# Optimization experiments

Measured on AMD Instinct MI355X. Metric: run time of the kernel, lower is better.

Reference implementation:

```python
import jax, jax.numpy as jnp
from jax import lax
import numpy as np

SCALES = 3
DIR_PROFILE = [2, 3, 4]


def _gaussian_lowpass():
    ks, sigma = 5, 1.0
    ax = np.arange(-ks // 2 + 1.0, ks // 2 + 1.0)
    g = np.exp(-0.5 * np.square(ax) / sigma ** 2)
    k1 = g / g.sum()
    k2 = np.outer(k1, k1)
    k2 = k2 / k2.sum()
    return k2.astype(np.float32)  # [5, 5]


def _oriented_filter(angle, scale):
    size = 15
    sx, sy = 2.0 * scale, 0.5 * scale
    x = np.arange(-size // 2 + 1, size // 2 + 1)
    y = np.arange(-size // 2 + 1, size // 2 + 1)
    X, Y = np.meshgrid(x, y)
    Xr = X * np.cos(angle) - Y * np.sin(angle)
    Yr = X * np.sin(angle) + Y * np.cos(angle)
    k = np.exp(-0.5 * (Xr ** 2 / sx ** 2 + Yr ** 2 / sy ** 2)) * Xr / sx ** 2
    k = k - k.mean()
    n = np.linalg.norm(k)
    if n > 1e-6:
        k = k / n
    return k.astype(np.float32)  # [15, 15]


LP_FILTER = jnp.asarray(_gaussian_lowpass())[None, None]  # [1,1,5,5]
DIR_FILTERS = []  # per scale: [n_dirs, 1, 15, 15]
for _s, _lvl in enumerate(DIR_PROFILE):
    _nd = 2 ** _lvl
    _fs = np.stack([_oriented_filter(np.pi * d / _nd, _s + 1) for d in range(_nd)])
    DIR_FILTERS.append(jnp.asarray(_fs)[:, None])


def _depthwise(x, kernel):
    # x: [N, 1, H, W]; kernel: [O, 1, kh, kw]; reflect-pad 'same' cross-correlation
    kh, kw = kernel.shape[2], kernel.shape[3]
    xp = jnp.pad(x, ((0, 0), (0, 0), (kh // 2, kh // 2), (kw // 2, kw // 2)), mode='reflect')
    return lax.conv_general_dilated(xp, kernel, (1, 1), 'VALID',
                                    dimension_numbers=('NCHW', 'OIHW', 'NCHW'))


def setup_inputs() -> dict:
    key = jax.random.key(0)
    x = jax.random.normal(key, (8, 3, 384, 384), dtype=jnp.float32)
    return {"x": x}


def reference(x) -> jnp.ndarray:
    B, C, H, W = x.shape
    xc = x.reshape(B * C, 1, H, W)  # each RGB channel processed independently

    # Non-subsampled Laplacian pyramid: bandpasses + final lowpass
    bandpasses = []
    current = xc
    for _ in range(SCALES):
        lp = _depthwise(current, LP_FILTER)
        bandpasses.append(current - lp)
        current = lp

    # Directional filter bank per scale (all directions in one grouped conv)
    feats = []
    for s in range(SCALES):
        feats.append(_depthwise(bandpasses[s], DIR_FILTERS[s]))  # [B*C, 2^lvl, H, W]
    feats.append(current)  # final lowpass [B*C, 1, H, W]

    out = jnp.concatenate(feats, axis=1)  # [B*C, 29, H, W]
    return out.reshape(B, C * out.shape[1], H, W)  # [B, 87, H, W]
```

## Files before the change

kernel.cpp:

```cpp
#include <hip/hip_runtime.h>

#define HH 384
#define WW 384
#define HWSZ (HH * WW)
#define NIMG 24

__device__ __forceinline__ int refl(int i, int n) {
    if (i < 0) i = -i;
    if (i >= n) i = 2 * n - 2 - i;
    return i;
}

constexpr float LPW[5] = {
    0.054488684549642945f, 0.24420134200323332f, 0.40261994689424746f,
    0.24420134200323332f, 0.054488684549642945f
};

constexpr double CPI = 3.141592653589793;

constexpr double cexp(double x) {
    int k = 0; double t = x;
    while (t > 0.25 || t < -0.25) { t *= 0.5; ++k; }
    double sum = 1.0, term = 1.0;
    for (int n = 1; n <= 14; ++n) { term *= t / n; sum += term; }
    for (int i = 0; i < k; ++i) sum *= sum;
    return sum;
}
constexpr double ccos(double x) {
    double sgn = 1.0;
    if (x > CPI * 0.5) { x = CPI - x; sgn = -1.0; }
    double x2 = x * x, sum = 1.0, term = 1.0;
    for (int n = 1; n <= 12; ++n) { term *= -x2 / ((2.0 * n - 1) * (2.0 * n)); sum += term; }
    return sgn * sum;
}
constexpr double csin(double x) {
    if (x > CPI * 0.5) x = CPI - x;
    double x2 = x * x, sum = x, term = x;
    for (int n = 1; n <= 12; ++n) { term *= -x2 / ((2.0 * n) * (2.0 * n + 1)); sum += term; }
    return sum;
}
constexpr double csqrt(double x) {
    if (x <= 0.0) return 0.0;
    double y = x > 1.0 ? x : 1.0;
    for (int i = 0; i < 80; ++i) y = 0.5 * (y + x / y);
    return y;
}

struct F225 { double v[225]; };

constexpr F225 make_filter(int s, int d, int nd) {
    double angle = CPI * (double)d / (double)nd;
    double scale = (double)(s + 1);
    double sx = 2.0 * scale, sy = 0.5 * scale;
    double ca = ccos(angle), sa = csin(angle);
    F225 f{};
    double sum = 0.0;
    for (int r = 0; r < 15; ++r)
        for (int c = 0; c < 15; ++c) {
            double X = (double)(c - 7), Y = (double)(r - 7);
            double Xr = X * ca - Y * sa;
            double Yr = X * sa + Y * ca;
            double k = cexp(-0.5 * (Xr * Xr / (sx * sx) + Yr * Yr / (sy * sy))) * Xr / (sx * sx);
            f.v[r * 15 + c] = k; sum += k;
        }
    double mean = sum / 225.0;
    double ss = 0.0;
    for (int i = 0; i < 225; ++i) { f.v[i] -= mean; ss += f.v[i] * f.v[i]; }
    double n = csqrt(ss);
    if (n > 1e-6) for (int i = 0; i < 225; ++i) f.v[i] /= n;
    return f;
}

template <int S, int D>
struct Filt { static constexpr F225 v = make_filter(S, D, S == 0 ? 4 : (S == 1 ? 8 : 16)); };

constexpr const F225& getF(int s, int d) {
    if (s == 0) {
        if (d == 0) return Filt<0, 0>::v;
        if (d == 1) return Filt<0, 1>::v;
        return Filt<0, 2>::v;
    } else if (s == 1) {
        if (d == 0) return Filt<1, 0>::v;
        if (d == 1) return Filt<1, 1>::v;
        if (d == 2) return Filt<1, 2>::v;
        if (d == 3) return Filt<1, 3>::v;
        return Filt<1, 4>::v;
    } else {
        if (d == 0) return Filt<2, 0>::v;
        if (d == 1) return Filt<2, 1>::v;
        if (d == 2) return Filt<2, 2>::v;
        if (d == 3) return Filt<2, 3>::v;
        if (d == 4) return Filt<2, 4>::v;
        if (d == 5) return Filt<2, 5>::v;
        if (d == 6) return Filt<2, 6>::v;
        if (d == 7) return Filt<2, 7>::v;
        return Filt<2, 8>::v;
    }
}

template <int NH> struct PTab { float a[63 * NH]; float b[63 * NH]; };

template <int NH>
constexpr PTab<NH> make_ptab(int s) {
    PTab<NH> t{};
    for (int j = 0; j < 63; ++j) {
        int u, v;
        if (j < 7)       { u = 0;     v = j + 1; }
        else if (j < 14) { u = j - 6; v = 0;     }
        else { int p = j - 14; u = p / 7 + 1; v = p % 7 + 1; }
        for (int k = 0; k < NH; ++k) {
            int dP = (k == 0) ? NH : k;
            int dQ = (k == 0) ? 0 : k;
            const F225& FP = getF(s, dP);
            const F225& FQ = getF(s, dQ);
            double A = 0.5 * (FP.v[(7 + u) * 15 + (7 + v)] + FP.v[(7 + u) * 15 + (7 - v)]);
            double B = 0.5 * (FQ.v[(7 + u) * 15 + (7 + v)] - FQ.v[(7 + u) * 15 + (7 - v)]);
            t.a[j * NH + k] = (float)A;
            t.b[j * NH + k] = (float)B;
        }
    }
    return t;
}
template <int S, int NH>
struct PTbl { static constexpr PTab<NH> t = make_ptab<NH>(S); };

template <int SIDX, int NH, int U>
struct UStep {
    static __device__ __forceinline__ void run(
        const float* sm, int yb, int xc, float (&accP)[NH], float (&accQ)[NH]) {
        {
            float dvc = sm[(yb + U) * 48 + xc] - sm[(yb - U) * 48 + xc];
#pragma unroll
            for (int k = 0; k < NH; ++k)
                accP[k] = fmaf(PTbl<SIDX, NH>::t.a[(6 + U) * NH + k], dvc, accP[k]);
        }
#pragma unroll
        for (int v = 1; v <= 7; ++v) {
            float a_ = sm[(yb + U) * 48 + xc + v];
            float b_ = sm[(yb + U) * 48 + xc - v];
            float c_ = sm[(yb - U) * 48 + xc + v];
            float d_ = sm[(yb - U) * 48 + xc - v];
            float t1 = a_ - d_, t2 = b_ - c_;
            float S = t1 + t2, D = t1 - t2;
#pragma unroll
            for (int k = 0; k < NH; ++k) {
                accP[k] = fmaf(PTbl<SIDX, NH>::t.a[(14 + (U - 1) * 7 + (v - 1)) * NH + k], S, accP[k]);
                accQ[k] = fmaf(PTbl<SIDX, NH>::t.b[(14 + (U - 1) * 7 + (v - 1)) * NH + k], D, accQ[k]);
            }
        }
        asm volatile("" ::: "memory");
        UStep<SIDX, NH, U + 1>::run(sm, yb, xc, accP, accQ);
    }
};
template <int SIDX, int NH>
struct UStep<SIDX, NH, 8> {
    static __device__ __forceinline__ void run(
        const float*, int, int, float (&)[NH], float (&)[NH]) {}
};

template <int SIDX, int NH>
__device__ __forceinline__ void dir_band(
    const float* sm, float* __restrict__ out, long nbase,
    int by, int bx, int tx, int ty, int c0) {
#pragma unroll 1
    for (int rr = 0; rr < 4; ++rr) {
        int yb = ty + 8 * rr + 7, xc = tx + 7;
        float accP[NH], accQ[NH];
#pragma unroll
        for (int k = 0; k < NH; ++k) { accP[k] = 0.f; accQ[k] = 0.f; }

#pragma unroll
        for (int v = 1; v <= 7; ++v) {
            float dv = sm[yb * 48 + xc + v] - sm[yb * 48 + xc - v];
#pragma unroll
            for (int k = 0; k < NH; ++k)
                accQ[k] = fmaf(PTbl<SIDX, NH>::t.b[(v - 1) * NH + k], dv, accQ[k]);
        }
        asm volatile("" ::: "memory");

        UStep<SIDX, NH, 1>::run(sm, yb, xc, accP, accQ);

        long idx = nbase + (long)c0 * HWSZ + (long)(by + ty + 8 * rr) * WW + bx + tx;
        out[idx] = accQ[0];
        out[idx + (long)NH * HWSZ] = accP[0];
#pragma unroll
        for (int k = 1; k < NH; ++k) {
            out[idx + (long)k * HWSZ] = accP[k] + accQ[k];
            out[idx + (long)(2 * NH - k) * HWSZ] = accP[k] - accQ[k];
        }
    }
}

__global__ __launch_bounds__(256, 4) void nsst_fused(
    const float* __restrict__ x, float* __restrict__ out) {
    __shared__ float Xb[58 * 60];
    __shared__ float Tb[58 * 56];
    __shared__ float Pb[54 * 56];

    int n = blockIdx.z;
    int bx = blockIdx.x * 32, by = blockIdx.y * 32;
    int tx = threadIdx.x, ty = threadIdx.y;
    int tid = ty * 32 + tx;
    const float* ip = x + (long)n * HWSZ;
    long nbase = (long)n * 29 * HWSZ;

    for (int l = tid; l < 58 * 58; l += 256) {
        int r = l / 58, c = l % 58;
        Xb[r * 60 + c] = ip[(long)refl(by + r - 13, HH) * WW + refl(bx + c - 13, WW)];
    }
    __syncthreads();
    for (int l = tid; l < 58 * 54; l += 256) {
        int r = l / 54, c = l % 54;
        float s = 0.f;
#pragma unroll
        for (int i = 0; i < 5; ++i) s = fmaf(LPW[i], Xb[r * 60 + c + i], s);
        Tb[r * 56 + c] = s;
    }
    __syncthreads();
    for (int l = tid; l < 54 * 54; l += 256) {
        int r = l / 54, c = l % 54;
        float s = 0.f;
#pragma unroll
        for (int i = 0; i < 5; ++i) s = fmaf(LPW[i], Tb[(r + i) * 56 + c], s);
        Pb[r * 56 + c] = s;
    }
    __syncthreads();
    for (int l = tid; l < 46 * 46; l += 256) {
        int r = l / 46, c = l % 46;
        Tb[r * 48 + c] = Xb[(r + 6) * 60 + c + 6] - Pb[(r + 4) * 56 + c + 4];
    }
    __syncthreads();
    dir_band<0, 2>(Tb, out, nbase, by, bx, tx, ty, 0);
    __syncthreads();
    for (int l = tid; l < 54 * 50; l += 256) {
        int r = l / 50, c = l % 50;
        float s = 0.f;
#pragma unroll
        for (int i = 0; i < 5; ++i) s = fmaf(LPW[i], Pb[r * 56 + c + i], s);
        Tb[r * 52 + c] = s;
    }
    __syncthreads();
    for (int l = tid; l < 50 * 50; l += 256) {
        int r = l / 50, c = l % 50;
        float s = 0.f;
#pragma unroll
        for (int i = 0; i < 5; ++i) s = fmaf(LPW[i], Tb[(r + i) * 52 + c], s);
        Xb[r * 52 + c] = s;
    }
    __syncthreads();
    for (int l = tid; l < 46 * 46; l += 256) {
        int r = l / 46, c = l % 46;
        Tb[r * 48 + c] = Pb[(r + 4) * 56 + c + 4] - Xb[(r + 2) * 52 + c + 2];
    }
    __syncthreads();
    dir_band<1, 4>(Tb, out, nbase, by, bx, tx, ty, 4);
    __syncthreads();
    for (int l = tid; l < 50 * 46; l += 256) {
        int r = l / 46, c = l % 46;
        float s = 0.f;
#pragma unroll
        for (int i = 0; i < 5; ++i) s = fmaf(LPW[i], Xb[r * 52 + c + i], s);
        Tb[r * 48 + c] = s;
    }
    __syncthreads();
    for (int l = tid; l < 46 * 46; l += 256) {
        int r = l / 46, c = l % 46;
        float s = 0.f;
#pragma unroll
        for (int i = 0; i < 5; ++i) s = fmaf(LPW[i], Tb[(r + i) * 48 + c], s);
        Pb[r * 48 + c] = s;
    }
    __syncthreads();
#pragma unroll
    for (int rr = 0; rr < 4; ++rr)
        out[nbase + 28l * HWSZ + (long)(by + ty + 8 * rr) * WW + bx + tx] =
            Pb[(ty + 8 * rr + 7) * 48 + tx + 7];
    for (int l = tid; l < 46 * 46; l += 256) {
        int r = l / 46, c = l % 46;
        Tb[r * 48 + c] = Xb[(r + 2) * 52 + c + 2] - Pb[r * 48 + c];
    }
    __syncthreads();
    dir_band<2, 8>(Tb, out, nbase, by, bx, tx, ty, 12);
}

extern "C" void kernel_launch(void* const* d_in, const int* in_sizes, int n_in,
                              void* d_out, int out_size, void* d_ws, size_t ws_size,
                              hipStream_t stream) {
    const float* x = (const float*)d_in[0];
    float* out = (float*)d_out;
    (void)d_ws; (void)ws_size;

    nsst_fused<<<dim3(12, 12, NIMG), dim3(32, 8), 0, stream>>>(x, out);
}
```

Baseline: 594.2 us.

## Compute two adjacent pixels per thread with inline-constant FMACs in directional filter

The directional filter bank now has each thread compute two horizontally adjacent output pixels over two row passes instead of one pixel over four. It loads pairs of shared-memory values and reuses each filter coefficient for both pixels through inline-asm v_fmac_f32 with literal constants, so table constants need no registers or loads. The bandpass tile stride changes from 48 to 49, likely to spread LDS banks, and the index-division loops for the lowpass stages are replaced by 2D row/column loops. The cost is doubled accumulator register pressure, up to 32 accumulators at the 8-direction scale, which may hurt occupancy under launch_bounds(256,4). The global stores are also now strided by two per lane.

```diff
diff --git a/kernel.cpp b/kernel.cpp
--- a/kernel.cpp
+++ b/kernel.cpp
@@ -4,6 +4,8 @@
 #define WW 384
 #define HWSZ (HH * WW)
 #define NIMG 24
+
+typedef float v2f __attribute__((ext_vector_type(2)));
 
 __device__ __forceinline__ int refl(int i, int n) {
     if (i < 0) i = -i;
@@ -124,69 +126,112 @@
 template <int S, int NH>
 struct PTbl { static constexpr PTab<NH> t = make_ptab<NH>(S); };
 
-template <int SIDX, int NH, int U>
-struct UStep {
-    static __device__ __forceinline__ void run(
-        const float* sm, int yb, int xc, float (&accP)[NH], float (&accQ)[NH]) {
+__device__ __forceinline__ v2f ld2(const float* p) {
+    v2f r; r.x = p[0]; r.y = p[1]; return r;
+}
+
+constexpr unsigned fb(float f) { return __builtin_bit_cast(unsigned, f); }
+
+template <unsigned B>
+__device__ __forceinline__ void fmac(float& a, float s) {
+    asm("v_fmac_f32 %0, %2, %1" : "+v"(a) : "v"(s), "n"(B));
+}
+
+template <int SIDX, int NH, int J, int K = 0>
+__device__ __forceinline__ void accA(float (&P0)[NH], float (&P1)[NH],
+                                     float sx, float sy) {
+    if constexpr (K < NH) {
+        constexpr unsigned b = fb(PTbl<SIDX, NH>::t.a[J * NH + K]);
+        fmac<b>(P0[K], sx);
+        fmac<b>(P1[K], sy);
+        accA<SIDX, NH, J, K + 1>(P0, P1, sx, sy);
+    }
+}
+template <int SIDX, int NH, int J, int K = 0>
+__device__ __forceinline__ void accB(float (&Q0)[NH], float (&Q1)[NH],
+                                     float dx, float dy) {
+    if constexpr (K < NH) {
+        constexpr unsigned b = fb(PTbl<SIDX, NH>::t.b[J * NH + K]);
+        fmac<b>(Q0[K], dx);
+        fmac<b>(Q1[K], dy);
+        accB<SIDX, NH, J, K + 1>(Q0, Q1, dx, dy);
+    }
+}
+
+template <int SIDX, int NH, int V = 1>
+__device__ __forceinline__ void runH0(const float* r0,
+                                      float (&Q0)[NH], float (&Q1)[NH]) {
+    if constexpr (V <= 7) {
+        v2f dv = ld2(r0 + V) - ld2(r0 - V);
+        accB<SIDX, NH, V - 1>(Q0, Q1, dv.x, dv.y);
+        runH0<SIDX, NH, V + 1>(r0, Q0, Q1);
+    }
+}
+
+template <int SIDX, int NH, int U, int V = 1>
+__device__ __forceinline__ void runV(const float* rp, const float* rm,
+                                     float (&P0)[NH], float (&Q0)[NH],
+                                     float (&P1)[NH], float (&Q1)[NH]) {
+    if constexpr (V <= 7) {
+        v2f a = ld2(rp + V);
+        v2f b = ld2(rp - V);
+        v2f c = ld2(rm + V);
+        v2f d = ld2(rm - V);
+        v2f t1 = a - d, t2 = b - c;
+        v2f S = t1 + t2, D = t1 - t2;
+        constexpr int J = 14 + (U - 1) * 7 + (V - 1);
+        accA<SIDX, NH, J>(P0, P1, S.x, S.y);
+        accB<SIDX, NH, J>(Q0, Q1, D.x, D.y);
+        runV<SIDX, NH, U, V + 1>(rp, rm, P0, Q0, P1, Q1);
+    }
+}
+
+template <int SIDX, int NH, int U = 1>
+__device__ __forceinline__ void runU(const float* sm, int yb, int xc,
+                                     float (&P0)[NH], float (&Q0)[NH],
+                                     float (&P1)[NH], float (&Q1)[NH]) {
+    if constexpr (U <= 7) {
+        const float* rp = sm + (yb + U) * 49 + xc;
+        const float* rm = sm + (yb - U) * 49 + xc;
         {
-            float dvc = sm[(yb + U) * 48 + xc] - sm[(yb - U) * 48 + xc];
-#pragma unroll
-            for (int k = 0; k < NH; ++k)
-                accP[k] = fmaf(PTbl<SIDX, NH>::t.a[(6 + U) * NH + k], dvc, accP[k]);
-        }
-#pragma unroll
-        for (int v = 1; v <= 7; ++v) {
-            float a_ = sm[(yb + U) * 48 + xc + v];
-            float b_ = sm[(yb + U) * 48 + xc - v];
-            float c_ = sm[(yb - U) * 48 + xc + v];
-            float d_ = sm[(yb - U) * 48 + xc - v];
-            float t1 = a_ - d_, t2 = b_ - c_;
-            float S = t1 + t2, D = t1 - t2;
-#pragma unroll
-            for (int k = 0; k < NH; ++k) {
-                accP[k] = fmaf(PTbl<SIDX, NH>::t.a[(14 + (U - 1) * 7 + (v - 1)) * NH + k], S, accP[k]);
-                accQ[k] = fmaf(PTbl<SIDX, NH>::t.b[(14 + (U - 1) * 7 + (v - 1)) * NH + k], D, accQ[k]);
-            }
-        }
+            v2f dvc = ld2(rp) - ld2(rm);
+            accA<SIDX, NH, 6 + U>(P0, P1, dvc.x, dvc.y);
+        }
+        runV<SIDX, NH, U>(rp, rm, P0, Q0, P1, Q1);
         asm volatile("" ::: "memory");
-        UStep<SIDX, NH, U + 1>::run(sm, yb, xc, accP, accQ);
-    }
-};
-template <int SIDX, int NH>
-struct UStep<SIDX, NH, 8> {
-    static __device__ __forceinline__ void run(
-        const float*, int, int, float (&)[NH], float (&)[NH]) {}
-};
+        runU<SIDX, NH, U + 1>(sm, yb, xc, P0, Q0, P1, Q1);
+    }
+}
 
 template <int SIDX, int NH>
 __device__ __forceinline__ void dir_band(
     const float* sm, float* __restrict__ out, long nbase,
-    int by, int bx, int tx, int ty, int c0) {
+    int by, int bx, int lane, int c0) {
+    int xg = (lane & 15) * 2;
+    int yr = lane >> 4;
+    int xc = xg + 7;
 #pragma unroll 1
-    for (int rr = 0; rr < 4; ++rr) {
-        int yb = ty + 8 * rr + 7, xc = tx + 7;
-        float accP[NH], accQ[NH];
-#pragma unroll
-        for (int k = 0; k < NH; ++k) { accP[k] = 0.f; accQ[k] = 0.f; }
-
-#pragma unroll
-        for (int v = 1; v <= 7; ++v) {
-            float dv = sm[yb * 48 + xc + v] - sm[yb * 48 + xc - v];
-#pragma unroll
-            for (int k = 0; k < NH; ++k)
-                accQ[k] = fmaf(PTbl<SIDX, NH>::t.b[(v - 1) * NH + k], dv, accQ[k]);
-        }
+    for (int rr = 0; rr < 2; ++rr) {
+        int yb = yr + 16 * rr + 7;
+        float P0[NH], Q0[NH], P1[NH], Q1[NH];
+#pragma unroll
+        for (int k = 0; k < NH; ++k) { P0[k] = 0.f; Q0[k] = 0.f; P1[k] = 0.f; Q1[k] = 0.f; }
+
+        runH0<SIDX, NH>(sm + yb * 49 + xc, Q0, Q1);
         asm volatile("" ::: "memory");
-
-        UStep<SIDX, NH, 1>::run(sm, yb, xc, accP, accQ);
-
-        long idx = nbase + (long)c0 * HWSZ + (long)(by + ty + 8 * rr) * WW + bx + tx;
-        out[idx] = accQ[0];
-        out[idx + (long)NH * HWSZ] = accP[0];
+        runU<SIDX, NH>(sm, yb, xc, P0, Q0, P1, Q1);
+
+        long idx = nbase + (long)c0 * HWSZ + (long)(by + yr + 16 * rr) * WW + bx + xg;
+        out[idx] = Q0[0];
+        out[idx + 1] = Q1[0];
+        out[idx + (long)NH * HWSZ] = P0[0];
+        out[idx + (long)NH * HWSZ + 1] = P1[0];
 #pragma unroll
         for (int k = 1; k < NH; ++k) {
-            out[idx + (long)k * HWSZ] = accP[k] + accQ[k];
-            out[idx + (long)(2 * NH - k) * HWSZ] = accP[k] - accQ[k];
+            out[idx + (long)k * HWSZ] = P0[k] + Q0[k];
+            out[idx + (long)k * HWSZ + 1] = P1[k] + Q1[k];
+            out[idx + (long)(2 * NH - k) * HWSZ] = P0[k] - Q0[k];
+            out[idx + (long)(2 * NH - k) * HWSZ + 1] = P1[k] - Q1[k];
         }
     }
 }
@@ -200,87 +245,85 @@
     int n = blockIdx.z;
     int bx = blockIdx.x * 32, by = blockIdx.y * 32;
     int tx = threadIdx.x, ty = threadIdx.y;
-    int tid = ty * 32 + tx;
+    int lane = ty * 32 + tx;
     const float* ip = x + (long)n * HWSZ;
     long nbase = (long)n * 29 * HWSZ;
 
-    for (int l = tid; l < 58 * 58; l += 256) {
-        int r = l / 58, c = l % 58;
-        Xb[r * 60 + c] = ip[(long)refl(by + r - 13, HH) * WW + refl(bx + c - 13, WW)];
-    }
-    __syncthreads();
-    for (int l = tid; l < 58 * 54; l += 256) {
-        int r = l / 54, c = l % 54;
-        float s = 0.f;
-#pragma unroll
-        for (int i = 0; i < 5; ++i) s = fmaf(LPW[i], Xb[r * 60 + c + i], s);
-        Tb[r * 56 + c] = s;
-    }
-    __syncthreads();
-    for (int l = tid; l < 54 * 54; l += 256) {
-        int r = l / 54, c = l % 54;
-        float s = 0.f;
-#pragma unroll
-        for (int i = 0; i < 5; ++i) s = fmaf(LPW[i], Tb[(r + i) * 56 + c], s);
-        Pb[r * 56 + c] = s;
-    }
-    __syncthreads();
-    for (int l = tid; l < 46 * 46; l += 256) {
-        int r = l / 46, c = l % 46;
-        Tb[r * 48 + c] = Xb[(r + 6) * 60 + c + 6] - Pb[(r + 4) * 56 + c + 4];
-    }
-    __syncthreads();
-    dir_band<0, 2>(Tb, out, nbase, by, bx, tx, ty, 0);
-    __syncthreads();
-    for (int l = tid; l < 54 * 50; l += 256) {
-        int r = l / 50, c = l % 50;
-        float s = 0.f;
-#pragma unroll
-        for (int i = 0; i < 5; ++i) s = fmaf(LPW[i], Pb[r * 56 + c + i], s);
-        Tb[r * 52 + c] = s;
-    }
-    __syncthreads();
-    for (int l = tid; l < 50 * 50; l += 256) {
-        int r = l / 50, c = l % 50;
-        float s = 0.f;
-#pragma unroll
-        for (int i = 0; i < 5; ++i) s = fmaf(LPW[i], Tb[(r + i) * 52 + c], s);
-        Xb[r * 52 + c] = s;
-    }
-    __syncthreads();
-    for (int l = tid; l < 46 * 46; l += 256) {
-        int r = l / 46, c = l % 46;
-        Tb[r * 48 + c] = Pb[(r + 4) * 56 + c + 4] - Xb[(r + 2) * 52 + c + 2];
-    }
-    __syncthreads();
-    dir_band<1, 4>(Tb, out, nbase, by, bx, tx, ty, 4);
-    __syncthreads();
-    for (int l = tid; l < 50 * 46; l += 256) {
-        int r = l / 46, c = l % 46;
-        float s = 0.f;
-#pragma unroll
-        for (int i = 0; i < 5; ++i) s = fmaf(LPW[i], Xb[r * 52 + c + i], s);
-        Tb[r * 48 + c] = s;
-    }
-    __syncthreads();
-    for (int l = tid; l < 46 * 46; l += 256) {
-        int r = l / 46, c = l % 46;
-        float s = 0.f;
-#pragma unroll
-        for (int i = 0; i < 5; ++i) s = fmaf(LPW[i], Tb[(r + i) * 48 + c], s);
-        Pb[r * 48 + c] = s;
-    }
+    for (int r = ty; r < 58; r += 8) {
+        int gy = refl(by + r - 13, HH);
+        for (int c = tx; c < 58; c += 32)
+            Xb[r * 60 + c] = ip[(long)gy * WW + refl(bx + c - 13, WW)];
+    }
+    __syncthreads();
+    for (int r = ty; r < 58; r += 8)
+        for (int c = tx; c < 54; c += 32) {
+            float s = 0.f;
+#pragma unroll
+            for (int i = 0; i < 5; ++i) s = fmaf(LPW[i], Xb[r * 60 + c + i], s);
+            Tb[r * 56 + c] = s;
+        }
+    __syncthreads();
+    for (int r = ty; r < 54; r += 8)
+        for (int c = tx; c < 54; c += 32) {
+            float s = 0.f;
+#pragma unroll
+            for (int i = 0; i < 5; ++i) s = fmaf(LPW[i], Tb[(r + i) * 56 + c], s);
+            Pb[r * 56 + c] = s;
+        }
+    __syncthreads();
+    for (int r = ty; r < 46; r += 8)
+        for (int c = tx; c < 46; c += 32)
+            Tb[r * 49 + c] = Xb[(r + 6) * 60 + c + 6] - Pb[(r + 4) * 56 + c + 4];
+    __syncthreads();
+    dir_band<0, 2>(Tb, out, nbase, by, bx, lane, 0);
+    __syncthreads();
+    for (int r = ty; r < 54; r += 8)
+        for (int c = tx; c < 50; c += 32) {
+            float s = 0.f;
+#pragma unroll
+            for (int i = 0; i < 5; ++i) s = fmaf(LPW[i], Pb[r * 56 + c + i], s);
+            Tb[r * 52 + c] = s;
+        }
+    __syncthreads();
+    for (int r = ty; r < 50; r += 8)
+        for (int c = tx; c < 50; c += 32) {
+            float s = 0.f;
+#pragma unroll
+            for (int i = 0; i < 5; ++i) s = fmaf(LPW[i], Tb[(r + i) * 52 + c], s);
+            Xb[r * 52 + c] = s;
+        }
+    __syncthreads();
+    for (int r = ty; r < 46; r += 8)
+        for (int c = tx; c < 46; c += 32)
+            Tb[r * 49 + c] = Pb[(r + 4) * 56 + c + 4] - Xb[(r + 2) * 52 + c + 2];
+    __syncthreads();
+    dir_band<1, 4>(Tb, out, nbase, by, bx, lane, 4);
+    __syncthreads();
+    for (int r = ty; r < 50; r += 8)
+        for (int c = tx; c < 46; c += 32) {
+            float s = 0.f;
+#pragma unroll
+            for (int i = 0; i < 5; ++i) s = fmaf(LPW[i], Xb[r * 52 + c + i], s);
+            Tb[r * 48 + c] = s;
+        }
+    __syncthreads();
+    for (int r = ty; r < 46; r += 8)
+        for (int c = tx; c < 46; c += 32) {
+            float s = 0.f;
+#pragma unroll
+            for (int i = 0; i < 5; ++i) s = fmaf(LPW[i], Tb[(r + i) * 48 + c], s);
+            Pb[r * 48 + c] = s;
+        }
     __syncthreads();
 #pragma unroll
     for (int rr = 0; rr < 4; ++rr)
         out[nbase + 28l * HWSZ + (long)(by + ty + 8 * rr) * WW + bx + tx] =
             Pb[(ty + 8 * rr + 7) * 48 + tx + 7];
-    for (int l = tid; l < 46 * 46; l += 256) {
-        int r = l / 46, c = l % 46;
-        Tb[r * 48 + c] = Xb[(r + 2) * 52 + c + 2] - Pb[r * 48 + c];
-    }
-    __syncthreads();
-    dir_band<2, 8>(Tb, out, nbase, by, bx, tx, ty, 12);
+    for (int r = ty; r < 46; r += 8)
+        for (int c = tx; c < 46; c += 32)
+            Tb[r * 49 + c] = Xb[(r + 2) * 52 + c + 2] - Pb[r * 48 + c];
+    __syncthreads();
+    dir_band<2, 8>(Tb, out, nbase, by, bx, lane, 12);
 }
 
 extern "C" void kernel_launch(void* const* d_in, const int* in_sizes, int n_in,
```

After: 558.5 us. 6.0% less time.
